# Optimization experiments

Measured on AMD Instinct MI355X. Metric: run time of the kernel, lower is better.

Reference implementation:

```python
import jax, jax.numpy as jnp
import numpy as np
import math

H = 768      # hidden_dim
NH = 12      # nhead
HD = H // NH # head_dim
FF = 4 * H
B, N = 8, 1024


def _layernorm(x, g, b, eps=1e-5):
    m = jnp.mean(x, axis=-1, keepdims=True)
    v = jnp.var(x, axis=-1, keepdims=True)
    return (x - m) * jax.lax.rsqrt(v + eps) * g + b


def setup_inputs() -> dict:
    key = jax.random.key(0)
    ks = jax.random.split(key, 16)
    s = 1.0 / math.sqrt(H)
    inp = {
        'x': jax.random.normal(ks[0], (B, N, H), jnp.float32),
        'attn_bias': jax.random.normal(ks[1], (NH, N, N), jnp.float32),
        'Wq': jax.random.normal(ks[2], (H, H), jnp.float32) * s,
        'bq': jnp.zeros((H,), jnp.float32),
        'Wk': jax.random.normal(ks[3], (H, H), jnp.float32) * s,
        'bk': jnp.zeros((H,), jnp.float32),
        'Wv': jax.random.normal(ks[4], (H, H), jnp.float32) * s,
        'bv': jnp.zeros((H,), jnp.float32),
        'Wo': jax.random.normal(ks[5], (H, H), jnp.float32) * s,
        'bo': jnp.zeros((H,), jnp.float32),
        'g1': jnp.ones((H,), jnp.float32),
        'be1': jnp.zeros((H,), jnp.float32),
        'W1': jax.random.normal(ks[6], (H, FF), jnp.float32) * s,
        'bf1': jnp.zeros((FF,), jnp.float32),
        'W2': jax.random.normal(ks[7], (FF, H), jnp.float32) * (1.0 / math.sqrt(FF)),
        'bf2': jnp.zeros((H,), jnp.float32),
        'g2': jnp.ones((H,), jnp.float32),
        'be2': jnp.zeros((H,), jnp.float32),
    }
    return inp


def reference(x, attn_bias, Wq, bq, Wk, bk, Wv, bv, Wo, bo, g1, be1, W1, bf1, W2, bf2, g2, be2):
    # dropout in eval mode (identity)
    Bc, Nc, C = x.shape
    q = (x @ Wq + bq).reshape(Bc, Nc, NH, HD).transpose(0, 2, 1, 3)  # [B,H,N,D]
    k = (x @ Wk + bk).reshape(Bc, Nc, NH, HD).transpose(0, 2, 1, 3)
    v = (x @ Wv + bv).reshape(Bc, Nc, NH, HD).transpose(0, 2, 1, 3)
    scores = jnp.einsum('bhnd,bhmd->bhnm', q, k) / math.sqrt(HD)
    scores = scores + attn_bias[None]  # bias broadcast over batch
    probs = jax.nn.softmax(scores, axis=-1)
    out = jnp.einsum('bhnm,bhmd->bhnd', probs, v)
    out = out.transpose(0, 2, 1, 3).reshape(Bc, Nc, C)
    out = out @ Wo + bo
    x = _layernorm(x + out, g1, be1)
    h = jax.nn.gelu(x @ W1 + bf1, approximate=False) @ W2 + bf2
    x = _layernorm(x + h, g2, be2)
    return x
```

## Files before the change

kernel.cpp:

```cpp
#include <hip/hip_runtime.h>
#include <math.h>

#define NH 12
#define HD 64
#define SEQ 1024
#define BATCH 8
#define HDIM 768
#define FFDIM 3072
#define MTOT (BATCH*SEQ)

typedef __attribute__((ext_vector_type(8))) short short8;
typedef __attribute__((ext_vector_type(4))) float f32x4;
typedef __attribute__((ext_vector_type(4))) unsigned short ushort4v;

__device__ __forceinline__ unsigned short f2b(float f) {
    union { float f; unsigned u; } v; v.f = f;
    unsigned r = v.u + 0x7fffu + ((v.u >> 16) & 1u);
    return (unsigned short)(r >> 16);
}

__device__ __forceinline__ f32x4 mfma16(short8 a, short8 b, f32x4 c) {
    return __builtin_amdgcn_mfma_f32_16x16x32_bf16(a, b, c, 0, 0, 0);
}

__device__ __forceinline__ void async_copy16(const unsigned short* g, unsigned short* l) {
    __builtin_amdgcn_global_load_lds(
        (const __attribute__((address_space(1))) unsigned int*)(const void*)g,
        (__attribute__((address_space(3))) unsigned int*)(void*)l, 16, 0, 0);
}

__global__ __launch_bounds__(256) void k_cvt(const float* __restrict__ in,
                                             unsigned short* __restrict__ out, int n) {
    int idx = (blockIdx.x * 256 + threadIdx.x) * 4;
    if (idx >= n) return;
    float4 v = *reinterpret_cast<const float4*>(in + idx);
    ushort4v o;
    o[0] = f2b(v.x); o[1] = f2b(v.y); o[2] = f2b(v.z); o[3] = f2b(v.w);
    *reinterpret_cast<ushort4v*>(out + idx) = o;
}

__global__ __launch_bounds__(256) void k_wt4(const float* __restrict__ W0,
                                             const float* __restrict__ W1,
                                             const float* __restrict__ W2,
                                             const float* __restrict__ W3,
                                             unsigned short* __restrict__ WT) {
    __shared__ float t[32][33];
    const float* W = (blockIdx.z == 0) ? W0 : (blockIdx.z == 1) ? W1 :
                     (blockIdx.z == 2) ? W2 : W3;
    unsigned short* dst = WT + (size_t)blockIdx.z * 768 * 768;
    int n0 = blockIdx.x * 32, k0 = blockIdx.y * 32;
    int x = threadIdx.x & 31, y = threadIdx.x >> 5;
#pragma unroll
    for (int i = y; i < 32; i += 8) t[i][x] = W[(size_t)(k0 + i) * 768 + n0 + x];
    __syncthreads();
#pragma unroll
    for (int i = y; i < 32; i += 8) dst[(size_t)(n0 + i) * 768 + k0 + x] = f2b(t[x][i]);
}

__global__ __launch_bounds__(256) void k_wt(const float* __restrict__ W,
                                            unsigned short* __restrict__ WT, int K, int Nn) {
    __shared__ float t[32][33];
    int n0 = blockIdx.x * 32, k0 = blockIdx.y * 32;
    int x = threadIdx.x & 31, y = threadIdx.x >> 5;
#pragma unroll
    for (int i = y; i < 32; i += 8) t[i][x] = W[(size_t)(k0 + i) * Nn + n0 + x];
    __syncthreads();
#pragma unroll
    for (int i = y; i < 32; i += 8) WT[(size_t)(n0 + i) * K + k0 + x] = f2b(t[x][i]);
}

__global__ void k_bias3(const float* __restrict__ a, const float* __restrict__ b,
                        const float* __restrict__ c, float* __restrict__ o) {
    int i = blockIdx.x * 256 + threadIdx.x;
    if (i >= 3 * HDIM) return;
    o[i] = (i < HDIM) ? a[i] : (i < 2 * HDIM ? b[i - HDIM] : c[i - 2 * HDIM]);
}

template<int EPI>
__global__ __launch_bounds__(256) void k_gemm(const unsigned short* __restrict__ A,
                                              const unsigned short* __restrict__ BT,
                                              const float* __restrict__ bias,
                                              const float* __restrict__ resid,
                                              unsigned short* __restrict__ outb,
                                              float* __restrict__ outf,
                                              int Mdim, int Ndim, int Kdim) {
    __shared__ unsigned short As[128 * 64];
    __shared__ unsigned short Bs[128 * 64];
    int tid = threadIdx.x;
    int wid = tid >> 6, lane = tid & 63;
    int wm = wid >> 1, wn = wid & 1;
    int l15 = lane & 15, l16 = lane >> 4;
    int bm = blockIdx.x * 128, bn = blockIdx.y * 128;

    int srow = wid * 8 + (lane >> 3);
    int scol = 8 * ((lane & 7) ^ (lane >> 3));
    const unsigned short* aptr = A + (size_t)(bm + srow) * Kdim + scol;
    const unsigned short* bptr = BT + (size_t)(bn + srow) * Kdim + scol;

    f32x4 acc[4][4] = {};
    const int swz = (l15 & 7) << 3;

    for (int kt = 0; kt < Kdim; kt += 64) {
#pragma unroll
        for (int c = 0; c < 4; c++) {
            async_copy16(aptr + (size_t)c * 32 * Kdim + kt, As + c * 2048 + wid * 512);
            async_copy16(bptr + (size_t)c * 32 * Kdim + kt, Bs + c * 2048 + wid * 512);
        }
        __syncthreads();
        short8 af[2][4], bfr[2][4];
#pragma unroll
        for (int kk = 0; kk < 2; kk++)
#pragma unroll
            for (int i = 0; i < 4; i++) {
                int ra = wm * 64 + i * 16 + l15;
                int rb = wn * 64 + i * 16 + l15;
                int cidx = (kk * 32 + l16 * 8) ^ swz;
                af[kk][i]  = *reinterpret_cast<const short8*>(&As[ra * 64 + cidx]);
                bfr[kk][i] = *reinterpret_cast<const short8*>(&Bs[rb * 64 + cidx]);
            }
#pragma unroll
        for (int kk = 0; kk < 2; kk++)
#pragma unroll
            for (int i = 0; i < 4; i++)
#pragma unroll
                for (int j = 0; j < 4; j++)
                    acc[i][j] = mfma16(af[kk][i], bfr[kk][j], acc[i][j]);
        __syncthreads();
    }

#pragma unroll
    for (int i = 0; i < 4; i++) {
#pragma unroll
        for (int j = 0; j < 4; j++) {
            int grow0 = bm + wm * 64 + i * 16 + l16 * 4;
            int gcol = bn + wn * 64 + j * 16 + l15;
            float bcol = bias[gcol];
#pragma unroll
            for (int r = 0; r < 4; r++) {
                int grow = grow0 + r;
                float v = acc[i][j][r] + bcol;
                size_t oi = (size_t)grow * Ndim + gcol;
                if constexpr (EPI == 0) {
                    outb[oi] = f2b(v);
                } else if constexpr (EPI == 1) {
                    outf[oi] = v + resid[oi];
                } else {
                    float g = 0.5f * v * (1.0f + erff(v * 0.70710678118654752f));
                    outb[oi] = f2b(g);
                }
            }
        }
    }
}

__global__ __launch_bounds__(256) void k_attn(const unsigned short* __restrict__ QKV,
                                              const float* __restrict__ bias,
                                              unsigned short* __restrict__ out) {
    __shared__ unsigned short Ks[64][72];
    __shared__ unsigned short Vt[64][72];
    __shared__ unsigned short Ps[4][16][72];

    int bh = blockIdx.y;
    int b = bh / NH, h = bh % NH;
    int q0 = blockIdx.x * 64;
    int tid = threadIdx.x, wid = tid >> 6, lane = tid & 63;
    int l15 = lane & 15, l16 = lane >> 4;

    size_t qrow = (size_t)(b * SEQ + q0 + wid * 16 + l15) * 2304 + h * 64;
    short8 qf0 = *reinterpret_cast<const short8*>(&QKV[qrow + l16 * 8]);
    short8 qf1 = *reinterpret_cast<const short8*>(&QKV[qrow + 32 + l16 * 8]);

    f32x4 o[4] = {};
    float mrow[4], lrow[4];
#pragma unroll
    for (int r = 0; r < 4; r++) { mrow[r] = -1e30f; lrow[r] = 0.0f; }

    for (int kt = 0; kt < SEQ; kt += 64) {
#pragma unroll
        for (int it = 0; it < 2; ++it) {
            int idx = tid + it * 256;
            int r = idx >> 3, c8 = (idx & 7) * 8;
            size_t gr = (size_t)(b * SEQ + kt + r) * 2304 + h * 64;
            *reinterpret_cast<short8*>(&Ks[r][c8]) =
                *reinterpret_cast<const short8*>(&QKV[gr + 768 + c8]);
            short8 vv = *reinterpret_cast<const short8*>(&QKV[gr + 1536 + c8]);
            int cc = r ^ c8;
#pragma unroll
            for (int j = 0; j < 8; j++) Vt[c8 + j][cc] = (unsigned short)vv[j];
        }
        __syncthreads();

        f32x4 s[4];
#pragma unroll
        for (int c = 0; c < 4; c++) {
            f32x4 t = {};
            t = mfma16(qf0, *reinterpret_cast<const short8*>(&Ks[c * 16 + l15][l16 * 8]), t);
            t = mfma16(qf1, *reinterpret_cast<const short8*>(&Ks[c * 16 + l15][32 + l16 * 8]), t);
            s[c] = t;
        }
#pragma unroll
        for (int c = 0; c < 4; c++)
#pragma unroll
            for (int r = 0; r < 4; r++) {
                size_t bi = (size_t)h * SEQ * SEQ +
                            (size_t)(q0 + wid * 16 + l16 * 4 + r) * SEQ + kt + c * 16 + l15;
                s[c][r] = s[c][r] * 0.125f + bias[bi];
            }
#pragma unroll
        for (int r = 0; r < 4; r++) {
            float mx = fmaxf(fmaxf(s[0][r], s[1][r]), fmaxf(s[2][r], s[3][r]));
#pragma unroll
            for (int off = 1; off < 16; off <<= 1) mx = fmaxf(mx, __shfl_xor(mx, off, 64));
            float mnew = fmaxf(mrow[r], mx);
            float resc = __expf(mrow[r] - mnew);
            mrow[r] = mnew;
            float sum = 0.0f;
#pragma unroll
            for (int c = 0; c < 4; c++) {
                float p = __expf(s[c][r] - mnew);
                s[c][r] = p; sum += p;
            }
#pragma unroll
            for (int off = 1; off < 16; off <<= 1) sum += __shfl_xor(sum, off, 64);
            lrow[r] = lrow[r] * resc + sum;
#pragma unroll
            for (int dc = 0; dc < 4; dc++) o[dc][r] *= resc;
        }
#pragma unroll
        for (int c = 0; c < 4; c++)
#pragma unroll
            for (int r = 0; r < 4; r++)
                Ps[wid][l16 * 4 + r][c * 16 + l15] = f2b(s[c][r]);
#pragma unroll
        for (int dc = 0; dc < 4; dc++) {
            int d = dc * 16 + l15;
            int sw = ((d >> 3) & 7) << 3;
#pragma unroll
            for (int kk = 0; kk < 2; kk++) {
                short8 pa = *reinterpret_cast<const short8*>(&Ps[wid][l15][kk * 32 + l16 * 8]);
                short8 vb = *reinterpret_cast<const short8*>(&Vt[d][(kk * 32 + l16 * 8) ^ sw]);
                o[dc] = mfma16(pa, vb, o[dc]);
            }
        }
        __syncthreads();
    }

#pragma unroll
    for (int dc = 0; dc < 4; dc++)
#pragma unroll
        for (int r = 0; r < 4; r++) {
            float v = o[dc][r] / lrow[r];
            size_t row = (size_t)(b * SEQ + q0 + wid * 16 + l16 * 4 + r);
            out[row * 768 + h * 64 + dc * 16 + l15] = f2b(v);
        }
}

template<int WB>
__global__ __launch_bounds__(256) void k_ln(const float* __restrict__ in,
                                            const float* __restrict__ gw,
                                            const float* __restrict__ bw,
                                            float* __restrict__ outf,
                                            unsigned short* __restrict__ outb) {
    int row = blockIdx.x, tid = threadIdx.x;
    const float* x = in + (size_t)row * 768;
    float v0 = x[tid], v1 = x[tid + 256], v2 = x[tid + 512];
    float s = v0 + v1 + v2;
    float s2 = v0 * v0 + v1 * v1 + v2 * v2;
#pragma unroll
    for (int off = 32; off; off >>= 1) {
        s += __shfl_down(s, off, 64);
        s2 += __shfl_down(s2, off, 64);
    }
    __shared__ float red[16];
    if ((tid & 63) == 0) { red[tid >> 6] = s; red[8 + (tid >> 6)] = s2; }
    __syncthreads();
    float ssum = red[0] + red[1] + red[2] + red[3];
    float s2sum = red[8] + red[9] + red[10] + red[11];
    float mean = ssum * (1.0f / 768.0f);
    float var = s2sum * (1.0f / 768.0f) - mean * mean;
    float rstd = rsqrtf(var + 1e-5f);
    float* of = outf + (size_t)row * 768;
    unsigned short* ob = outb ? outb + (size_t)row * 768 : nullptr;
    float vv[3] = { v0, v1, v2 };
#pragma unroll
    for (int i = 0; i < 3; i++) {
        int col = tid + i * 256;
        float y = (vv[i] - mean) * rstd * gw[col] + bw[col];
        of[col] = y;
        if constexpr (WB) ob[col] = f2b(y);
    }
}

constexpr size_t OFF_XB    = 0;
constexpr size_t OFF_QKV   = OFF_XB    + 12582912;
constexpr size_t OFF_ATT   = OFF_QKV   + 37748736;
constexpr size_t OFF_WQKVT = OFF_ATT   + 12582912;
constexpr size_t OFF_WOT   = OFF_WQKVT + 3538944;
constexpr size_t OFF_W1T   = OFF_WOT   + 1179648;
constexpr size_t OFF_W2T   = OFF_W1T   + 4718592;
constexpr size_t OFF_BQKV  = OFF_W2T   + 4718592;
constexpr size_t OFF_TMP   = OFF_BQKV  + 9216;
constexpr size_t OFF_X1F   = OFF_TMP   + 25165824;
constexpr size_t OFF_X1B   = OFF_X1F   + 25165824;
constexpr size_t OFF_H     = OFF_X1B   + 12582912;

extern "C" void kernel_launch(void* const* d_in, const int* in_sizes, int n_in,
                              void* d_out, int out_size, void* d_ws, size_t ws_size,
                              hipStream_t stream) {
    const float* x    = (const float*)d_in[0];
    const float* ab   = (const float*)d_in[1];
    const float* Wq   = (const float*)d_in[2];
    const float* bq   = (const float*)d_in[3];
    const float* Wk   = (const float*)d_in[4];
    const float* bk   = (const float*)d_in[5];
    const float* Wv   = (const float*)d_in[6];
    const float* bv   = (const float*)d_in[7];
    const float* Wo   = (const float*)d_in[8];
    const float* bo   = (const float*)d_in[9];
    const float* g1   = (const float*)d_in[10];
    const float* be1  = (const float*)d_in[11];
    const float* W1   = (const float*)d_in[12];
    const float* bf1  = (const float*)d_in[13];
    const float* W2   = (const float*)d_in[14];
    const float* bf2  = (const float*)d_in[15];
    const float* g2   = (const float*)d_in[16];
    const float* be2  = (const float*)d_in[17];

    char* ws = (char*)d_ws;
    unsigned short* xb    = (unsigned short*)(ws + OFF_XB);
    unsigned short* qkv   = (unsigned short*)(ws + OFF_QKV);
    unsigned short* att   = (unsigned short*)(ws + OFF_ATT);
    unsigned short* wqkvt = (unsigned short*)(ws + OFF_WQKVT);
    unsigned short* wot   = (unsigned short*)(ws + OFF_WOT);
    unsigned short* w1t   = (unsigned short*)(ws + OFF_W1T);
    unsigned short* w2t   = (unsigned short*)(ws + OFF_W2T);
    float*          bqkv  = (float*)(ws + OFF_BQKV);
    float*          tmp   = (float*)(ws + OFF_TMP);
    float*          x1f   = (float*)(ws + OFF_X1F);
    unsigned short* x1b   = (unsigned short*)(ws + OFF_X1B);
    unsigned short* hb    = (unsigned short*)(ws + OFF_H);
    float*          out   = (float*)d_out;

    k_cvt<<<dim3(MTOT * HDIM / 1024), dim3(256), 0, stream>>>(x, xb, MTOT * HDIM);
    k_wt4<<<dim3(24, 24, 4), dim3(256), 0, stream>>>(Wq, Wk, Wv, Wo, wqkvt);
    k_wt<<<dim3(96, 24), dim3(256), 0, stream>>>(W1, w1t, HDIM, FFDIM);
    k_wt<<<dim3(24, 96), dim3(256), 0, stream>>>(W2, w2t, FFDIM, HDIM);
    k_bias3<<<dim3(9), dim3(256), 0, stream>>>(bq, bk, bv, bqkv);

    k_gemm<0><<<dim3(64, 18), dim3(256), 0, stream>>>(xb, wqkvt, bqkv, nullptr, qkv, nullptr,
                                                      MTOT, 3 * HDIM, HDIM);
    k_attn<<<dim3(SEQ / 64, BATCH * NH), dim3(256), 0, stream>>>(qkv, ab, att);
    k_gemm<1><<<dim3(64, 6), dim3(256), 0, stream>>>(att, wot, bo, x, nullptr, tmp,
                                                     MTOT, HDIM, HDIM);
    k_ln<1><<<dim3(MTOT), dim3(256), 0, stream>>>(tmp, g1, be1, x1f, x1b);
    k_gemm<2><<<dim3(64, 24), dim3(256), 0, stream>>>(x1b, w1t, bf1, nullptr, hb, nullptr,
                                                      MTOT, FFDIM, HDIM);
    k_gemm<1><<<dim3(64, 6), dim3(256), 0, stream>>>(hb, w2t, bf2, x1f, nullptr, tmp,
                                                     MTOT, HDIM, FFDIM);
    k_ln<0><<<dim3(MTOT), dim3(256), 0, stream>>>(tmp, g2, be2, out, nullptr);
}
```

Measured before the change: 496.2 us.

## Use larger 512-thread GEMM tiles with XCD-aware block remapping

Adds a k_gemm8 kernel with 8 waves and 256-column tiles (256x256 or 128x256), used for the QKV, FFN1 and FFN2 GEMMs, to raise data reuse per LDS load. Blocks are remapped along the M dimension so that neighbouring tiles land on the same XCD and share L2. The k-loop now loads fragments per half-step, which lowers register pressure. The larger tiles leave fewer blocks (e.g. 192 for FFN2, 288 for QKV), which could underfill the 256 CUs, and the larger LDS and accumulator footprint lowers occupancy.

Result: slower. 534.7 us (+7.8%).

```diff
diff --git a/kernel.cpp b/kernel.cpp
--- a/kernel.cpp
+++ b/kernel.cpp
@@ -27,6 +27,10 @@
     __builtin_amdgcn_global_load_lds(
         (const __attribute__((address_space(1))) unsigned int*)(const void*)g,
         (__attribute__((address_space(3))) unsigned int*)(void*)l, 16, 0, 0);
+}
+
+__device__ __forceinline__ int xcd_remap_x(int gx, int GX) {
+    return ((GX & 7) == 0) ? (gx & 7) * (GX >> 3) + (gx >> 3) : gx;
 }
 
 __global__ __launch_bounds__(256) void k_cvt(const float* __restrict__ in,
@@ -77,20 +81,35 @@
 }
 
 template<int EPI>
+__device__ __forceinline__ void epi_store(float v, size_t oi,
+                                          unsigned short* outb, float* outf,
+                                          const float* resid) {
+    if constexpr (EPI == 0) {
+        outb[oi] = f2b(v);
+    } else if constexpr (EPI == 1) {
+        outf[oi] = v + resid[oi];
+    } else {
+        float g = 0.5f * v * (1.0f + erff(v * 0.70710678118654752f));
+        outb[oi] = f2b(g);
+    }
+}
+
+template<int EPI>
 __global__ __launch_bounds__(256) void k_gemm(const unsigned short* __restrict__ A,
                                               const unsigned short* __restrict__ BT,
                                               const float* __restrict__ bias,
                                               const float* __restrict__ resid,
                                               unsigned short* __restrict__ outb,
                                               float* __restrict__ outf,
-                                              int Mdim, int Ndim, int Kdim) {
+                                              int Ndim, int Kdim) {
     __shared__ unsigned short As[128 * 64];
     __shared__ unsigned short Bs[128 * 64];
     int tid = threadIdx.x;
     int wid = tid >> 6, lane = tid & 63;
     int wm = wid >> 1, wn = wid & 1;
     int l15 = lane & 15, l16 = lane >> 4;
-    int bm = blockIdx.x * 128, bn = blockIdx.y * 128;
+    int gx = xcd_remap_x(blockIdx.x, gridDim.x);
+    int bm = gx * 128, bn = blockIdx.y * 128;
 
     int srow = wid * 8 + (lane >> 3);
     int scol = 8 * ((lane & 7) ^ (lane >> 3));
@@ -107,50 +126,107 @@
             async_copy16(bptr + (size_t)c * 32 * Kdim + kt, Bs + c * 2048 + wid * 512);
         }
         __syncthreads();
-        short8 af[2][4], bfr[2][4];
-#pragma unroll
-        for (int kk = 0; kk < 2; kk++)
+#pragma unroll
+        for (int kk = 0; kk < 2; kk++) {
+            short8 af[4], bfr[4];
+            int cidx = (kk * 32 + l16 * 8) ^ swz;
 #pragma unroll
             for (int i = 0; i < 4; i++) {
-                int ra = wm * 64 + i * 16 + l15;
-                int rb = wn * 64 + i * 16 + l15;
-                int cidx = (kk * 32 + l16 * 8) ^ swz;
-                af[kk][i]  = *reinterpret_cast<const short8*>(&As[ra * 64 + cidx]);
-                bfr[kk][i] = *reinterpret_cast<const short8*>(&Bs[rb * 64 + cidx]);
+                af[i]  = *reinterpret_cast<const short8*>(&As[(wm * 64 + i * 16 + l15) * 64 + cidx]);
+                bfr[i] = *reinterpret_cast<const short8*>(&Bs[(wn * 64 + i * 16 + l15) * 64 + cidx]);
             }
 #pragma unroll
-        for (int kk = 0; kk < 2; kk++)
-#pragma unroll
             for (int i = 0; i < 4; i++)
 #pragma unroll
                 for (int j = 0; j < 4; j++)
-                    acc[i][j] = mfma16(af[kk][i], bfr[kk][j], acc[i][j]);
-        __syncthreads();
-    }
-
-#pragma unroll
-    for (int i = 0; i < 4; i++) {
+                    acc[i][j] = mfma16(af[i], bfr[j], acc[i][j]);
+        }
+        __syncthreads();
+    }
+
+#pragma unroll
+    for (int i = 0; i < 4; i++)
 #pragma unroll
         for (int j = 0; j < 4; j++) {
             int grow0 = bm + wm * 64 + i * 16 + l16 * 4;
             int gcol = bn + wn * 64 + j * 16 + l15;
             float bcol = bias[gcol];
 #pragma unroll
-            for (int r = 0; r < 4; r++) {
-                int grow = grow0 + r;
-                float v = acc[i][j][r] + bcol;
-                size_t oi = (size_t)grow * Ndim + gcol;
-                if constexpr (EPI == 0) {
-                    outb[oi] = f2b(v);
-                } else if constexpr (EPI == 1) {
-                    outf[oi] = v + resid[oi];
-                } else {
-                    float g = 0.5f * v * (1.0f + erff(v * 0.70710678118654752f));
-                    outb[oi] = f2b(g);
-                }
-            }
-        }
-    }
+            for (int r = 0; r < 4; r++)
+                epi_store<EPI>(acc[i][j][r] + bcol, (size_t)(grow0 + r) * Ndim + gcol,
+                               outb, outf, resid);
+        }
+}
+
+template<int MT, int EPI>
+__global__ __launch_bounds__(512, 2) void k_gemm8(const unsigned short* __restrict__ A,
+                                                  const unsigned short* __restrict__ BT,
+                                                  const float* __restrict__ bias,
+                                                  const float* __restrict__ resid,
+                                                  unsigned short* __restrict__ outb,
+                                                  float* __restrict__ outf,
+                                                  int Ndim, int Kdim) {
+    constexpr int BM = MT * 32;
+    __shared__ unsigned short As[BM * 64];
+    __shared__ unsigned short Bs[256 * 64];
+    int tid = threadIdx.x;
+    int wid = tid >> 6, lane = tid & 63;
+    int wm = wid >> 2, wn = wid & 3;
+    int l15 = lane & 15, l16 = lane >> 4;
+    int gx = xcd_remap_x(blockIdx.x, gridDim.x);
+    int bm = gx * BM, bn = blockIdx.y * 256;
+
+    int srow = (tid >> 3) & 7;
+    int srow_full = wid * 8 + (lane >> 3);
+    int scol = 8 * ((lane & 7) ^ (lane >> 3));
+    const unsigned short* aptr = A + (size_t)(bm + srow_full) * Kdim + scol;
+    const unsigned short* bptr = BT + (size_t)(bn + srow_full) * Kdim + scol;
+    (void)srow;
+
+    f32x4 acc[MT][4] = {};
+    const int swz = (l15 & 7) << 3;
+
+    for (int kt = 0; kt < Kdim; kt += 64) {
+#pragma unroll
+        for (int c = 0; c < BM / 64; c++)
+            async_copy16(aptr + (size_t)c * 64 * Kdim + kt, As + c * 4096 + wid * 512);
+#pragma unroll
+        for (int c = 0; c < 4; c++)
+            async_copy16(bptr + (size_t)c * 64 * Kdim + kt, Bs + c * 4096 + wid * 512);
+        __syncthreads();
+#pragma unroll
+        for (int kk = 0; kk < 2; kk++) {
+            short8 af[MT], bfr[4];
+            int cidx = (kk * 32 + l16 * 8) ^ swz;
+#pragma unroll
+            for (int i = 0; i < MT; i++)
+                af[i] = *reinterpret_cast<const short8*>(
+                    &As[(wm * (MT * 16) + i * 16 + l15) * 64 + cidx]);
+#pragma unroll
+            for (int j = 0; j < 4; j++)
+                bfr[j] = *reinterpret_cast<const short8*>(
+                    &Bs[(wn * 64 + j * 16 + l15) * 64 + cidx]);
+#pragma unroll
+            for (int i = 0; i < MT; i++)
+#pragma unroll
+                for (int j = 0; j < 4; j++)
+                    acc[i][j] = mfma16(af[i], bfr[j], acc[i][j]);
+        }
+        __syncthreads();
+    }
+
+#pragma unroll
+    for (int i = 0; i < MT; i++)
+#pragma unroll
+        for (int j = 0; j < 4; j++) {
+            int grow0 = bm + wm * (MT * 16) + i * 16 + l16 * 4;
+            int gcol = bn + wn * 64 + j * 16 + l15;
+            float bcol = bias[gcol];
+#pragma unroll
+            for (int r = 0; r < 4; r++)
+                epi_store<EPI>(acc[i][j][r] + bcol, (size_t)(grow0 + r) * Ndim + gcol,
+                               outb, outf, resid);
+        }
 }
 
 __global__ __launch_bounds__(256) void k_attn(const unsigned short* __restrict__ QKV,
@@ -347,15 +423,15 @@
     k_wt<<<dim3(24, 96), dim3(256), 0, stream>>>(W2, w2t, FFDIM, HDIM);
     k_bias3<<<dim3(9), dim3(256), 0, stream>>>(bq, bk, bv, bqkv);
 
-    k_gemm<0><<<dim3(64, 18), dim3(256), 0, stream>>>(xb, wqkvt, bqkv, nullptr, qkv, nullptr,
-                                                      MTOT, 3 * HDIM, HDIM);
+    k_gemm8<8, 0><<<dim3(32, 9), dim3(512), 0, stream>>>(xb, wqkvt, bqkv, nullptr, qkv, nullptr,
+                                                         3 * HDIM, HDIM);
     k_attn<<<dim3(SEQ / 64, BATCH * NH), dim3(256), 0, stream>>>(qkv, ab, att);
     k_gemm<1><<<dim3(64, 6), dim3(256), 0, stream>>>(att, wot, bo, x, nullptr, tmp,
-                                                     MTOT, HDIM, HDIM);
+                                                     HDIM, HDIM);
     k_ln<1><<<dim3(MTOT), dim3(256), 0, stream>>>(tmp, g1, be1, x1f, x1b);
-    k_gemm<2><<<dim3(64, 24), dim3(256), 0, stream>>>(x1b, w1t, bf1, nullptr, hb, nullptr,
-                                                      MTOT, FFDIM, HDIM);
-    k_gemm<1><<<dim3(64, 6), dim3(256), 0, stream>>>(hb, w2t, bf2, x1f, nullptr, tmp,
-                                                     MTOT, HDIM, FFDIM);
+    k_gemm8<8, 2><<<dim3(32, 12), dim3(512), 0, stream>>>(x1b, w1t, bf1, nullptr, hb, nullptr,
+                                                          FFDIM, HDIM);
+    k_gemm8<4, 1><<<dim3(64, 3), dim3(512), 0, stream>>>(hb, w2t, bf2, x1f, nullptr, tmp,
+                                                         HDIM, FFDIM);
     k_ln<0><<<dim3(MTOT), dim3(256), 0, stream>>>(tmp, g2, be2, out, nullptr);
 }
```

## Pre-transpose V in a separate kernel and vectorize attention bias loads

Applied to the files above, without the earlier changes.

Adds a kernel that writes V transposed per (batch, head) into a scratch buffer, using a permuted key order. The attention kernel can then copy V^T tiles directly instead of doing scalar transposed LDS stores. K rows are loaded in the same permuted order, so each lane reads four consecutive bias values as one float4 instead of four scattered scalar loads. This costs an extra kernel launch and a round trip of V through global memory, and it reuses the tmp workspace region for V^T.

Result: no change. 495.5 us (-0.1%).

```diff
diff --git a/kernel.cpp b/kernel.cpp
--- a/kernel.cpp
+++ b/kernel.cpp
@@ -76,6 +76,49 @@
     o[i] = (i < HDIM) ? a[i] : (i < 2 * HDIM ? b[i - HDIM] : c[i - 2 * HDIM]);
 }
 
+__global__ __launch_bounds__(256) void k_vtr(const unsigned short* __restrict__ QKV,
+                                             unsigned short* __restrict__ VT) {
+    __shared__ unsigned short T[64][72];
+    int kt = blockIdx.x * 64;
+    int bh = blockIdx.y;
+    int b = bh / NH, h = bh % NH;
+    int tid = threadIdx.x;
+#pragma unroll
+    for (int it = 0; it < 2; ++it) {
+        int idx = tid + it * 256;
+        int r = idx >> 3, c8 = (idx & 7) * 8;
+        *reinterpret_cast<short8*>(&T[r][c8]) = *reinterpret_cast<const short8*>(
+            &QKV[(size_t)(b * SEQ + kt + r) * 2304 + 1536 + h * 64 + c8]);
+    }
+    __syncthreads();
+#pragma unroll
+    for (int it = 0; it < 2; ++it) {
+        int idx = tid + it * 256;
+        int d = idx >> 3, c8 = (idx & 7) * 8;
+        short8 o;
+#pragma unroll
+        for (int j = 0; j < 8; j++) {
+            int slot = c8 + j;
+            o[j] = (short)T[(slot & 15) * 4 + (slot >> 4)][d];
+        }
+        *reinterpret_cast<short8*>(&VT[((size_t)bh * 64 + d) * SEQ + kt + c8]) = o;
+    }
+}
+
+template<int EPI>
+__device__ __forceinline__ void epi_store(float v, size_t oi,
+                                          unsigned short* outb, float* outf,
+                                          const float* resid) {
+    if constexpr (EPI == 0) {
+        outb[oi] = f2b(v);
+    } else if constexpr (EPI == 1) {
+        outf[oi] = v + resid[oi];
+    } else {
+        float g = 0.5f * v * (1.0f + erff(v * 0.70710678118654752f));
+        outb[oi] = f2b(g);
+    }
+}
+
 template<int EPI>
 __global__ __launch_bounds__(256) void k_gemm(const unsigned short* __restrict__ A,
                                               const unsigned short* __restrict__ BT,
@@ -83,7 +126,7 @@
                                               const float* __restrict__ resid,
                                               unsigned short* __restrict__ outb,
                                               float* __restrict__ outf,
-                                              int Mdim, int Ndim, int Kdim) {
+                                              int Ndim, int Kdim) {
     __shared__ unsigned short As[128 * 64];
     __shared__ unsigned short Bs[128 * 64];
     int tid = threadIdx.x;
@@ -107,53 +150,40 @@
             async_copy16(bptr + (size_t)c * 32 * Kdim + kt, Bs + c * 2048 + wid * 512);
         }
         __syncthreads();
-        short8 af[2][4], bfr[2][4];
-#pragma unroll
-        for (int kk = 0; kk < 2; kk++)
+#pragma unroll
+        for (int kk = 0; kk < 2; kk++) {
+            short8 af[4], bfr[4];
+            int cidx = (kk * 32 + l16 * 8) ^ swz;
 #pragma unroll
             for (int i = 0; i < 4; i++) {
-                int ra = wm * 64 + i * 16 + l15;
-                int rb = wn * 64 + i * 16 + l15;
-                int cidx = (kk * 32 + l16 * 8) ^ swz;
-                af[kk][i]  = *reinterpret_cast<const short8*>(&As[ra * 64 + cidx]);
-                bfr[kk][i] = *reinterpret_cast<const short8*>(&Bs[rb * 64 + cidx]);
+                af[i]  = *reinterpret_cast<const short8*>(&As[(wm * 64 + i * 16 + l15) * 64 + cidx]);
+                bfr[i] = *reinterpret_cast<const short8*>(&Bs[(wn * 64 + i * 16 + l15) * 64 + cidx]);
             }
 #pragma unroll
-        for (int kk = 0; kk < 2; kk++)
-#pragma unroll
             for (int i = 0; i < 4; i++)
 #pragma unroll
                 for (int j = 0; j < 4; j++)
-                    acc[i][j] = mfma16(af[kk][i], bfr[kk][j], acc[i][j]);
+                    acc[i][j] = mfma16(af[i], bfr[j], acc[i][j]);
+        }
         __syncthreads();
     }
 
 #pragma unroll
-    for (int i = 0; i < 4; i++) {
+    for (int i = 0; i < 4; i++)
 #pragma unroll
         for (int j = 0; j < 4; j++) {
             int grow0 = bm + wm * 64 + i * 16 + l16 * 4;
             int gcol = bn + wn * 64 + j * 16 + l15;
             float bcol = bias[gcol];
 #pragma unroll
-            for (int r = 0; r < 4; r++) {
-                int grow = grow0 + r;
-                float v = acc[i][j][r] + bcol;
-                size_t oi = (size_t)grow * Ndim + gcol;
-                if constexpr (EPI == 0) {
-                    outb[oi] = f2b(v);
-                } else if constexpr (EPI == 1) {
-                    outf[oi] = v + resid[oi];
-                } else {
-                    float g = 0.5f * v * (1.0f + erff(v * 0.70710678118654752f));
-                    outb[oi] = f2b(g);
-                }
-            }
-        }
-    }
+            for (int r = 0; r < 4; r++)
+                epi_store<EPI>(acc[i][j][r] + bcol, (size_t)(grow0 + r) * Ndim + gcol,
+                               outb, outf, resid);
+        }
 }
 
 __global__ __launch_bounds__(256) void k_attn(const unsigned short* __restrict__ QKV,
+                                              const unsigned short* __restrict__ VT,
                                               const float* __restrict__ bias,
                                               unsigned short* __restrict__ out) {
     __shared__ unsigned short Ks[64][72];
@@ -170,6 +200,9 @@
     short8 qf0 = *reinterpret_cast<const short8*>(&QKV[qrow + l16 * 8]);
     short8 qf1 = *reinterpret_cast<const short8*>(&QKV[qrow + 32 + l16 * 8]);
 
+    const float* brow = bias + (size_t)h * SEQ * SEQ +
+                        (size_t)(q0 + wid * 16 + l16 * 4) * SEQ;
+
     f32x4 o[4] = {};
     float mrow[4], lrow[4];
 #pragma unroll
@@ -180,13 +213,11 @@
         for (int it = 0; it < 2; ++it) {
             int idx = tid + it * 256;
             int r = idx >> 3, c8 = (idx & 7) * 8;
-            size_t gr = (size_t)(b * SEQ + kt + r) * 2304 + h * 64;
-            *reinterpret_cast<short8*>(&Ks[r][c8]) =
-                *reinterpret_cast<const short8*>(&QKV[gr + 768 + c8]);
-            short8 vv = *reinterpret_cast<const short8*>(&QKV[gr + 1536 + c8]);
-            int cc = r ^ c8;
-#pragma unroll
-            for (int j = 0; j < 8; j++) Vt[c8 + j][cc] = (unsigned short)vv[j];
+            int pr = (r & 15) * 4 + (r >> 4);
+            *reinterpret_cast<short8*>(&Ks[r][c8]) = *reinterpret_cast<const short8*>(
+                &QKV[(size_t)(b * SEQ + kt + pr) * 2304 + 768 + h * 64 + c8]);
+            *reinterpret_cast<short8*>(&Vt[r][c8]) = *reinterpret_cast<const short8*>(
+                &VT[((size_t)bh * 64 + r) * SEQ + kt + c8]);
         }
         __syncthreads();
 
@@ -199,13 +230,13 @@
             s[c] = t;
         }
 #pragma unroll
-        for (int c = 0; c < 4; c++)
-#pragma unroll
-            for (int r = 0; r < 4; r++) {
-                size_t bi = (size_t)h * SEQ * SEQ +
-                            (size_t)(q0 + wid * 16 + l16 * 4 + r) * SEQ + kt + c * 16 + l15;
-                s[c][r] = s[c][r] * 0.125f + bias[bi];
-            }
+        for (int r = 0; r < 4; r++) {
+            float4 bv = *reinterpret_cast<const float4*>(&brow[(size_t)r * SEQ + kt + l15 * 4]);
+            s[0][r] = s[0][r] * 0.125f + bv.x;
+            s[1][r] = s[1][r] * 0.125f + bv.y;
+            s[2][r] = s[2][r] * 0.125f + bv.z;
+            s[3][r] = s[3][r] * 0.125f + bv.w;
+        }
 #pragma unroll
         for (int r = 0; r < 4; r++) {
             float mx = fmaxf(fmaxf(s[0][r], s[1][r]), fmaxf(s[2][r], s[3][r]));
@@ -234,11 +265,10 @@
 #pragma unroll
         for (int dc = 0; dc < 4; dc++) {
             int d = dc * 16 + l15;
-            int sw = ((d >> 3) & 7) << 3;
 #pragma unroll
             for (int kk = 0; kk < 2; kk++) {
                 short8 pa = *reinterpret_cast<const short8*>(&Ps[wid][l15][kk * 32 + l16 * 8]);
-                short8 vb = *reinterpret_cast<const short8*>(&Vt[d][(kk * 32 + l16 * 8) ^ sw]);
+                short8 vb = *reinterpret_cast<const short8*>(&Vt[d][kk * 32 + l16 * 8]);
                 o[dc] = mfma16(pa, vb, o[dc]);
             }
         }
@@ -336,6 +366,7 @@
     unsigned short* w2t   = (unsigned short*)(ws + OFF_W2T);
     float*          bqkv  = (float*)(ws + OFF_BQKV);
     float*          tmp   = (float*)(ws + OFF_TMP);
+    unsigned short* vt    = (unsigned short*)(ws + OFF_TMP);
     float*          x1f   = (float*)(ws + OFF_X1F);
     unsigned short* x1b   = (unsigned short*)(ws + OFF_X1B);
     unsigned short* hb    = (unsigned short*)(ws + OFF_H);
@@ -348,14 +379,15 @@
     k_bias3<<<dim3(9), dim3(256), 0, stream>>>(bq, bk, bv, bqkv);
 
     k_gemm<0><<<dim3(64, 18), dim3(256), 0, stream>>>(xb, wqkvt, bqkv, nullptr, qkv, nullptr,
-                                                      MTOT, 3 * HDIM, HDIM);
-    k_attn<<<dim3(SEQ / 64, BATCH * NH), dim3(256), 0, stream>>>(qkv, ab, att);
+                                                      3 * HDIM, HDIM);
+    k_vtr<<<dim3(SEQ / 64, BATCH * NH), dim3(256), 0, stream>>>(qkv, vt);
+    k_attn<<<dim3(SEQ / 64, BATCH * NH), dim3(256), 0, stream>>>(qkv, vt, ab, att);
     k_gemm<1><<<dim3(64, 6), dim3(256), 0, stream>>>(att, wot, bo, x, nullptr, tmp,
-                                                     MTOT, HDIM, HDIM);
+                                                     HDIM, HDIM);
     k_ln<1><<<dim3(MTOT), dim3(256), 0, stream>>>(tmp, g1, be1, x1f, x1b);
     k_gemm<2><<<dim3(64, 24), dim3(256), 0, stream>>>(x1b, w1t, bf1, nullptr, hb, nullptr,
-                                                      MTOT, FFDIM, HDIM);
+                                                      FFDIM, HDIM);
     k_gemm<1><<<dim3(64, 6), dim3(256), 0, stream>>>(hb, w2t, bf2, x1f, nullptr, tmp,
-                                                     MTOT, HDIM, FFDIM);
+                                                     HDIM, FFDIM);
     k_ln<0><<<dim3(MTOT), dim3(256), 0, stream>>>(tmp, g2, be2, out, nullptr);
 }
```
